# Kernel tuning notes

Measured on AMD Instinct MI355X. Metric: run time of the kernel, lower is better.

## Reference

```python
import jax, jax.numpy as jnp
import numpy as np

LMAX, RB, RA, N, D = 4, 12, 11, 131072, 64
S = (LMAX + 1) ** 2


def _assoc_legendre_norm(lmax, x):
    # Fully-normalized associated Legendre P_l^m(x), orthonormal over the sphere
    # (includes sqrt((2l+1)/(4pi) * (l-m)!/(l+m)!)). x: [B] = cos(beta).
    B = x.shape[0]
    s = np.sqrt(np.clip(1.0 - x * x, 0.0, 1.0))
    P = np.zeros((lmax + 1, lmax + 1, B))
    P[0, 0] = np.sqrt(1.0 / (4.0 * np.pi))
    for m in range(1, lmax + 1):
        P[m, m] = -np.sqrt((2.0 * m + 1.0) / (2.0 * m)) * s * P[m - 1, m - 1]
    for m in range(0, lmax):
        P[m + 1, m] = np.sqrt(2.0 * m + 3.0) * x * P[m, m]
    for m in range(0, lmax + 1):
        for l in range(m + 2, lmax + 1):
            a = np.sqrt((4.0 * l * l - 1.0) / (l * l - m * m))
            b = np.sqrt((((l - 1) ** 2 - m * m)) / (4.0 * (l - 1) ** 2 - 1.0))
            P[l, m] = a * (x * P[l - 1, m] - b * P[l - 2, m])
    return P


def _sh_grid(lmax, res_beta, res_alpha):
    # Real orthonormal spherical harmonics sampled on a Gauss-Legendre x uniform-alpha grid,
    # plus quadrature weights so that sum_{b,a} Y_i Y_j qw_b = delta_ij (band-limited).
    x, w = np.polynomial.legendre.leggauss(res_beta)  # nodes in cos(beta)
    alpha = 2.0 * np.pi * np.arange(res_alpha) / res_alpha
    P = _assoc_legendre_norm(lmax, x)  # [L+1, L+1, RB]
    Ssz = (lmax + 1) ** 2
    Y = np.zeros((res_beta, res_alpha, Ssz))
    i = 0
    for l in range(lmax + 1):
        for m in range(-l, l + 1):
            if m < 0:
                ang = np.sqrt(2.0) * np.sin(-m * alpha)
            elif m == 0:
                ang = np.ones_like(alpha)
            else:
                ang = np.sqrt(2.0) * np.cos(m * alpha)
            Y[:, :, i] = P[l, abs(m)][:, None] * ang[None, :]
            i += 1
    qw = w * (2.0 * np.pi / res_alpha)  # beta quadrature * alpha trapezoid weight
    return Y.astype(np.float32), qw.astype(np.float32)


def setup_inputs() -> dict:
    key = jax.random.key(0)
    k1, k2, k3, k4 = jax.random.split(key, 4)
    Y_np, qw_np = _sh_grid(LMAX, RB, RA)
    Y = jnp.asarray(Y_np)                       # [RB, RA, S]
    Yw = Y * jnp.asarray(qw_np)[:, None, None]  # [RB, RA, S] (quadrature-weighted)
    input1 = jax.random.normal(k1, (N, D), dtype=jnp.float32)
    input2 = jax.random.normal(k2, (N, D), dtype=jnp.float32)
    W1 = jax.random.normal(k3, (D, S), dtype=jnp.float32) * 0.1
    W2 = jax.random.normal(k4, (D, S), dtype=jnp.float32) * 0.1
    return {"input1": input1, "input2": input2, "W1": W1, "W2": W2, "Y": Y, "Yw": Yw}


def reference(input1, input2, W1, W2, Y, Yw):
    # linear_in: project input irreps to S2 spherical-harmonic coefficients
    c1 = input1 @ W1  # [N, S]
    c2 = input2 @ W2  # [N, S]
    # ToS2Grid: evaluate band-limited signal on the (beta, alpha) grid
    g1 = jnp.einsum("ns,bas->nba", c1, Y)  # [N, RB, RA]
    g2 = jnp.einsum("ns,bas->nba", c2, Y)
    # pointwise product on the sphere, then FromS2Grid (quadrature projection)
    return jnp.einsum("nba,bas->ns", g1 * g2, Yw)  # [N, S]
```

## Files before the change

### kernel.cpp

```cpp
#include <hip/hip_runtime.h>


typedef __bf16 bf16x8 __attribute__((ext_vector_type(8)));
typedef float f32x4 __attribute__((ext_vector_type(4)));

namespace {
constexpr int kD = 64, kS = 25, kP = 132;
constexpr int kBlock = 256, kM = 128;
constexpr int kInStride = 72;
constexpr int kHStride = 168;
constexpr int kOffIn2 = kM * kInStride;
constexpr int kSmemU = kM * kHStride;
constexpr int kWsA2 = 9216, kWsB2 = 18432;
}

__device__ __forceinline__ unsigned short f2bf(float f) {
    unsigned int u = __builtin_bit_cast(unsigned int, f);
    u += 0x7FFFu + ((u >> 16) & 1u);
    return (unsigned short)(u >> 16);
}

__device__ __forceinline__ bf16x8 ld_frag_g(const unsigned short* p) {
    int4 v = *reinterpret_cast<const int4*>(p);
    return __builtin_bit_cast(bf16x8, v);
}

__global__ void precompute_kernel(const float* __restrict__ W1,
                                  const float* __restrict__ W2,
                                  const float* __restrict__ Y,
                                  const float* __restrict__ Yw,
                                  unsigned short* __restrict__ ws) {
    const int t0 = blockIdx.x * blockDim.x + threadIdx.x;
    const int stride = gridDim.x * blockDim.x;
    for (int e = t0; e < 9216; e += stride) {
        const int j = e & 7, lane = (e >> 3) & 63, ks = (e >> 9) & 1, nt = e >> 10;
        const int k = ks * 32 + (lane >> 4) * 8 + j;
        const int n = nt * 16 + (lane & 15);
        float v1 = 0.f, v2 = 0.f;
        if (n < kP) {
            const float* yr = Y + n * kS;
            const float* w1 = W1 + k * kS;
            const float* w2 = W2 + k * kS;
            #pragma unroll
            for (int s = 0; s < kS; ++s) {
                v1 = fmaf(w1[s], yr[s], v1);
                v2 = fmaf(w2[s], yr[s], v2);
            }
        }
        ws[e]         = f2bf(v1);
        ws[kWsA2 + e] = f2bf(v2);
    }
    for (int e = t0; e < 5120; e += stride) {
        const int j = e & 7, lane = (e >> 3) & 63, r = e >> 9;
        const int ks = r % 5, nt = r / 5;
        const int k = ks * 32 + (lane >> 4) * 8 + j;
        const int n = nt * 16 + (lane & 15);
        ws[kWsB2 + e] = (k < kP && n < kS) ? f2bf(Yw[k * kS + n]) : (unsigned short)0;
    }
}

__global__ __launch_bounds__(kBlock, 3) void gaunt_mfma(
    const float* __restrict__ in1, const float* __restrict__ in2,
    const unsigned short* __restrict__ ws, float* __restrict__ out)
{
    __shared__ unsigned short smem[kSmemU];
    const int tid  = threadIdx.x;
    const int lane = tid & 63;
    const int w    = __builtin_amdgcn_readfirstlane(tid >> 6);
    const int lo16 = lane & 15, quad = lane >> 4;

    const long long base = (long long)blockIdx.x * (kM * kD);
    const float4* __restrict__ g1v = reinterpret_cast<const float4*>(in1 + base);
    const float4* __restrict__ g2v = reinterpret_cast<const float4*>(in2 + base);
    #pragma unroll
    for (int i = 0; i < (kM * kD) / (4 * kBlock); ++i) {
        const int idx = i * kBlock + tid;
        const int row = idx >> 4, c4 = (idx & 15) * 4;
        const float4 v1 = g1v[idx];
        const float4 v2 = g2v[idx];
        ushort4 p1, p2;
        p1.x = f2bf(v1.x); p1.y = f2bf(v1.y); p1.z = f2bf(v1.z); p1.w = f2bf(v1.w);
        p2.x = f2bf(v2.x); p2.y = f2bf(v2.y); p2.z = f2bf(v2.z); p2.w = f2bf(v2.w);
        *reinterpret_cast<ushort4*>(&smem[row * kInStride + c4])          = p1;
        *reinterpret_cast<ushort4*>(&smem[kOffIn2 + row * kInStride + c4]) = p2;
    }
    __syncthreads();

    bf16x8 a1f[2][2], a2f[2][2];
    #pragma unroll
    for (int rt = 0; rt < 2; ++rt) {
        const int row = (2 * w + rt) * 16 + lo16;
        const int kbase = row * kInStride + quad * 8;
        #pragma unroll
        for (int ks = 0; ks < 2; ++ks) {
            a1f[rt][ks] = ld_frag_g(&smem[kbase + ks * 32]);
            a2f[rt][ks] = ld_frag_g(&smem[kOffIn2 + kbase + ks * 32]);
        }
    }
    __syncthreads();

    {
        const int r = tid >> 1, half = tid & 1;
        unsigned int* p =
            reinterpret_cast<unsigned int*>(&smem[r * kHStride + 144 + half * 12]);
        p[0] = 0u; p[1] = 0u; p[2] = 0u; p[3] = 0u; p[4] = 0u; p[5] = 0u;
    }

    const unsigned short* wsA1 = ws;
    const unsigned short* wsA2 = ws + kWsA2;
    bf16x8 b1c[2], b2c[2], b1n[2], b2n[2];
    #pragma unroll
    for (int ks = 0; ks < 2; ++ks) {
        b1c[ks] = ld_frag_g(&wsA1[(0 * 2 + ks) * 512 + lane * 8]);
        b2c[ks] = ld_frag_g(&wsA2[(0 * 2 + ks) * 512 + lane * 8]);
    }
    #pragma unroll 1
    for (int nt = 0; nt < 9; ++nt) {
        if (nt < 8) {
            #pragma unroll
            for (int ks = 0; ks < 2; ++ks) {
                b1n[ks] = ld_frag_g(&wsA1[((nt + 1) * 2 + ks) * 512 + lane * 8]);
                b2n[ks] = ld_frag_g(&wsA2[((nt + 1) * 2 + ks) * 512 + lane * 8]);
            }
        }
        f32x4 g1[2], g2[2];
        #pragma unroll
        for (int rt = 0; rt < 2; ++rt) {
            g1[rt] = (f32x4){0.f, 0.f, 0.f, 0.f};
            g2[rt] = (f32x4){0.f, 0.f, 0.f, 0.f};
            #pragma unroll
            for (int ks = 0; ks < 2; ++ks) {
                g1[rt] = __builtin_amdgcn_mfma_f32_16x16x32_bf16(
                    a1f[rt][ks], b1c[ks], g1[rt], 0, 0, 0);
                g2[rt] = __builtin_amdgcn_mfma_f32_16x16x32_bf16(
                    a2f[rt][ks], b2c[ks], g2[rt], 0, 0, 0);
            }
        }
        const int hcol = nt * 16 + lo16;
        #pragma unroll
        for (int rt = 0; rt < 2; ++rt) {
            #pragma unroll
            for (int i = 0; i < 4; ++i) {
                const int row = (2 * w + rt) * 16 + quad * 4 + i;
                smem[row * kHStride + hcol] = f2bf(g1[rt][i] * g2[rt][i]);
            }
        }
        #pragma unroll
        for (int ks = 0; ks < 2; ++ks) { b1c[ks] = b1n[ks]; b2c[ks] = b2n[ks]; }
    }
    __syncthreads();

    const unsigned short* wsB2 = ws + kWsB2;
    f32x4 o[2][2];
    #pragma unroll
    for (int rt = 0; rt < 2; ++rt)
        #pragma unroll
        for (int nt = 0; nt < 2; ++nt)
            o[rt][nt] = (f32x4){0.f, 0.f, 0.f, 0.f};

    bf16x8 bbc[2], bbn[2];
    #pragma unroll
    for (int nt = 0; nt < 2; ++nt)
        bbc[nt] = ld_frag_g(&wsB2[(nt * 5 + 0) * 512 + lane * 8]);

    #pragma unroll 1
    for (int ks = 0; ks < 5; ++ks) {
        if (ks < 4) {
            #pragma unroll
            for (int nt = 0; nt < 2; ++nt)
                bbn[nt] = ld_frag_g(&wsB2[(nt * 5 + ks + 1) * 512 + lane * 8]);
        }
        bf16x8 hf[2];
        #pragma unroll
        for (int rt = 0; rt < 2; ++rt) {
            const int row = (2 * w + rt) * 16 + lo16;
            hf[rt] = ld_frag_g(&smem[row * kHStride + ks * 32 + quad * 8]);
        }
        #pragma unroll
        for (int rt = 0; rt < 2; ++rt)
            #pragma unroll
            for (int nt = 0; nt < 2; ++nt)
                o[rt][nt] = __builtin_amdgcn_mfma_f32_16x16x32_bf16(
                    hf[rt], bbc[nt], o[rt][nt], 0, 0, 0);
        bbc[0] = bbn[0]; bbc[1] = bbn[1];
    }

    const long long ob = (long long)blockIdx.x * (kM * kS);
    #pragma unroll
    for (int rt = 0; rt < 2; ++rt) {
        #pragma unroll
        for (int nt = 0; nt < 2; ++nt) {
            const int col = nt * 16 + lo16;
            if (col < kS) {
                #pragma unroll
                for (int i = 0; i < 4; ++i) {
                    const int row = (2 * w + rt) * 16 + quad * 4 + i;
                    out[ob + row * kS + col] = o[rt][nt][i];
                }
            }
        }
    }
}

extern "C" void kernel_launch(void* const* d_in, const int* in_sizes, int n_in,
                              void* d_out, int out_size, void* d_ws, size_t ws_size,
                              hipStream_t stream) {
    const float* in1 = (const float*)d_in[0];
    const float* in2 = (const float*)d_in[1];
    const float* W1  = (const float*)d_in[2];
    const float* W2  = (const float*)d_in[3];
    const float* Y   = (const float*)d_in[4];
    const float* Yw  = (const float*)d_in[5];
    float* out = (float*)d_out;
    unsigned short* ws = (unsigned short*)d_ws;

    precompute_kernel<<<8, 256, 0, stream>>>(W1, W2, Y, Yw, ws);

    const int n_rows = in_sizes[0] / kD;
    const int grid = n_rows / kM;
    gaunt_mfma<<<grid, kBlock, 0, stream>>>(in1, in2, ws, out);
}
```

Measured before the change: 120.1 us.

## Load MFMA A-fragments directly from global memory and drop LDS staging and barriers

Inputs are now read straight from global memory into the registers that feed the A-fragments, converted to bf16 with native casts, instead of being staged through LDS with two __syncthreads. The barrier between the H write and the second GEMM is also removed, which is safe only because each wave reads back just the rows it wrote itself. The padding zeroing moves to the start of the kernel. This cuts LDS traffic and synchronisation at the cost of less coalesced global loads (each lane reads 32-byte pieces spread across rows).

```diff
diff --git a/kernel.cpp b/kernel.cpp
--- a/kernel.cpp
+++ b/kernel.cpp
@@ -7,9 +7,7 @@
 namespace {
 constexpr int kD = 64, kS = 25, kP = 132;
 constexpr int kBlock = 256, kM = 128;
-constexpr int kInStride = 72;
 constexpr int kHStride = 168;
-constexpr int kOffIn2 = kM * kInStride;
 constexpr int kSmemU = kM * kHStride;
 constexpr int kWsA2 = 9216, kWsB2 = 18432;
 }
@@ -23,6 +21,13 @@
 __device__ __forceinline__ bf16x8 ld_frag_g(const unsigned short* p) {
     int4 v = *reinterpret_cast<const int4*>(p);
     return __builtin_bit_cast(bf16x8, v);
+}
+
+__device__ __forceinline__ bf16x8 cvt8(f32x4 u, f32x4 v) {
+    bf16x8 r;
+    r[0] = (__bf16)u[0]; r[1] = (__bf16)u[1]; r[2] = (__bf16)u[2]; r[3] = (__bf16)u[3];
+    r[4] = (__bf16)v[0]; r[5] = (__bf16)v[1]; r[6] = (__bf16)v[2]; r[7] = (__bf16)v[3];
+    return r;
 }
 
 __global__ void precompute_kernel(const float* __restrict__ W1,
@@ -59,7 +64,7 @@
     }
 }
 
-__global__ __launch_bounds__(kBlock, 3) void gaunt_mfma(
+__global__ __launch_bounds__(kBlock, 3) void gaunt_mfma5(
     const float* __restrict__ in1, const float* __restrict__ in2,
     const unsigned short* __restrict__ ws, float* __restrict__ out)
 {
@@ -69,41 +74,27 @@
     const int w    = __builtin_amdgcn_readfirstlane(tid >> 6);
     const int lo16 = lane & 15, quad = lane >> 4;
 
+    {
+        const int r = tid >> 1, c = 144 + (tid & 1) * 8;
+        *reinterpret_cast<int4*>(&smem[r * kHStride + c]) = (int4){0, 0, 0, 0};
+    }
+
     const long long base = (long long)blockIdx.x * (kM * kD);
-    const float4* __restrict__ g1v = reinterpret_cast<const float4*>(in1 + base);
-    const float4* __restrict__ g2v = reinterpret_cast<const float4*>(in2 + base);
-    #pragma unroll
-    for (int i = 0; i < (kM * kD) / (4 * kBlock); ++i) {
-        const int idx = i * kBlock + tid;
-        const int row = idx >> 4, c4 = (idx & 15) * 4;
-        const float4 v1 = g1v[idx];
-        const float4 v2 = g2v[idx];
-        ushort4 p1, p2;
-        p1.x = f2bf(v1.x); p1.y = f2bf(v1.y); p1.z = f2bf(v1.z); p1.w = f2bf(v1.w);
-        p2.x = f2bf(v2.x); p2.y = f2bf(v2.y); p2.z = f2bf(v2.z); p2.w = f2bf(v2.w);
-        *reinterpret_cast<ushort4*>(&smem[row * kInStride + c4])          = p1;
-        *reinterpret_cast<ushort4*>(&smem[kOffIn2 + row * kInStride + c4]) = p2;
-    }
-    __syncthreads();
-
     bf16x8 a1f[2][2], a2f[2][2];
     #pragma unroll
     for (int rt = 0; rt < 2; ++rt) {
         const int row = (2 * w + rt) * 16 + lo16;
-        const int kbase = row * kInStride + quad * 8;
+        const float* p1 = in1 + base + row * kD + quad * 8;
+        const float* p2 = in2 + base + row * kD + quad * 8;
         #pragma unroll
         for (int ks = 0; ks < 2; ++ks) {
-            a1f[rt][ks] = ld_frag_g(&smem[kbase + ks * 32]);
-            a2f[rt][ks] = ld_frag_g(&smem[kOffIn2 + kbase + ks * 32]);
-        }
-    }
-    __syncthreads();
-
-    {
-        const int r = tid >> 1, half = tid & 1;
-        unsigned int* p =
-            reinterpret_cast<unsigned int*>(&smem[r * kHStride + 144 + half * 12]);
-        p[0] = 0u; p[1] = 0u; p[2] = 0u; p[3] = 0u; p[4] = 0u; p[5] = 0u;
+            const f32x4 u1 = *reinterpret_cast<const f32x4*>(p1 + ks * 32);
+            const f32x4 v1 = *reinterpret_cast<const f32x4*>(p1 + ks * 32 + 4);
+            const f32x4 u2 = *reinterpret_cast<const f32x4*>(p2 + ks * 32);
+            const f32x4 v2 = *reinterpret_cast<const f32x4*>(p2 + ks * 32 + 4);
+            a1f[rt][ks] = cvt8(u1, v1);
+            a2f[rt][ks] = cvt8(u2, v2);
+        }
     }
 
     const unsigned short* wsA1 = ws;
@@ -111,8 +102,8 @@
     bf16x8 b1c[2], b2c[2], b1n[2], b2n[2];
     #pragma unroll
     for (int ks = 0; ks < 2; ++ks) {
-        b1c[ks] = ld_frag_g(&wsA1[(0 * 2 + ks) * 512 + lane * 8]);
-        b2c[ks] = ld_frag_g(&wsA2[(0 * 2 + ks) * 512 + lane * 8]);
+        b1c[ks] = ld_frag_g(&wsA1[ks * 512 + lane * 8]);
+        b2c[ks] = ld_frag_g(&wsA2[ks * 512 + lane * 8]);
     }
     #pragma unroll 1
     for (int nt = 0; nt < 9; ++nt) {
@@ -123,32 +114,26 @@
                 b2n[ks] = ld_frag_g(&wsA2[((nt + 1) * 2 + ks) * 512 + lane * 8]);
             }
         }
-        f32x4 g1[2], g2[2];
         #pragma unroll
         for (int rt = 0; rt < 2; ++rt) {
-            g1[rt] = (f32x4){0.f, 0.f, 0.f, 0.f};
-            g2[rt] = (f32x4){0.f, 0.f, 0.f, 0.f};
+            f32x4 g1 = (f32x4){0.f, 0.f, 0.f, 0.f};
+            f32x4 g2 = (f32x4){0.f, 0.f, 0.f, 0.f};
             #pragma unroll
             for (int ks = 0; ks < 2; ++ks) {
-                g1[rt] = __builtin_amdgcn_mfma_f32_16x16x32_bf16(
-                    a1f[rt][ks], b1c[ks], g1[rt], 0, 0, 0);
-                g2[rt] = __builtin_amdgcn_mfma_f32_16x16x32_bf16(
-                    a2f[rt][ks], b2c[ks], g2[rt], 0, 0, 0);
-            }
-        }
-        const int hcol = nt * 16 + lo16;
-        #pragma unroll
-        for (int rt = 0; rt < 2; ++rt) {
+                g1 = __builtin_amdgcn_mfma_f32_16x16x32_bf16(a1f[rt][ks], b1c[ks], g1, 0, 0, 0);
+                g2 = __builtin_amdgcn_mfma_f32_16x16x32_bf16(a2f[rt][ks], b2c[ks], g2, 0, 0, 0);
+            }
+            const int hcol = nt * 16 + lo16;
             #pragma unroll
             for (int i = 0; i < 4; ++i) {
                 const int row = (2 * w + rt) * 16 + quad * 4 + i;
-                smem[row * kHStride + hcol] = f2bf(g1[rt][i] * g2[rt][i]);
+                smem[row * kHStride + hcol] =
+                    __builtin_bit_cast(unsigned short, (__bf16)(g1[i] * g2[i]));
             }
         }
         #pragma unroll
         for (int ks = 0; ks < 2; ++ks) { b1c[ks] = b1n[ks]; b2c[ks] = b2n[ks]; }
     }
-    __syncthreads();
 
     const unsigned short* wsB2 = ws + kWsB2;
     f32x4 o[2][2];
@@ -161,7 +146,7 @@
     bf16x8 bbc[2], bbn[2];
     #pragma unroll
     for (int nt = 0; nt < 2; ++nt)
-        bbc[nt] = ld_frag_g(&wsB2[(nt * 5 + 0) * 512 + lane * 8]);
+        bbc[nt] = ld_frag_g(&wsB2[(nt * 5) * 512 + lane * 8]);
 
     #pragma unroll 1
     for (int ks = 0; ks < 5; ++ks) {
@@ -174,7 +159,9 @@
         #pragma unroll
         for (int rt = 0; rt < 2; ++rt) {
             const int row = (2 * w + rt) * 16 + lo16;
-            hf[rt] = ld_frag_g(&smem[row * kHStride + ks * 32 + quad * 8]);
+            const int4 hv = *reinterpret_cast<const int4*>(
+                &smem[row * kHStride + ks * 32 + quad * 8]);
+            hf[rt] = __builtin_bit_cast(bf16x8, hv);
         }
         #pragma unroll
         for (int rt = 0; rt < 2; ++rt)
@@ -218,5 +205,5 @@
 
     const int n_rows = in_sizes[0] / kD;
     const int grid = n_rows / kM;
-    gaunt_mfma<<<grid, kBlock, 0, stream>>>(in1, in2, ws, out);
-}
+    gaunt_mfma5<<<grid, kBlock, 0, stream>>>(in1, in2, ws, out);
+}
```

New measurement: 118.0 us. No clear change (-1.8%).
